# Kernel optimization log

Measured on AMD Instinct MI355X. Metric: run time of the kernel, lower is better.

Reference implementation:

```python
import math
import jax, jax.numpy as jnp
import numpy as np

NUM_HEADS = 12
HEAD_DIM = 64
HIDDEN = NUM_HEADS * HEAD_DIM  # 768
SEQ = 4096


def setup_inputs() -> dict:
    key = jax.random.key(0)
    ks = jax.random.split(key, 7)
    s = 0.02  # BERT-style init scale for weights
    return {
        "hidden_states": jax.random.normal(ks[0], (1, SEQ, HIDDEN), jnp.float32),
        "Wq": jax.random.normal(ks[1], (HIDDEN, HIDDEN), jnp.float32) * s,
        "bq": jax.random.normal(ks[2], (HIDDEN,), jnp.float32) * s,
        "Wk": jax.random.normal(ks[3], (HIDDEN, HIDDEN), jnp.float32) * s,
        "bk": jax.random.normal(ks[4], (HIDDEN,), jnp.float32) * s,
        "Wv": jax.random.normal(ks[5], (HIDDEN, HIDDEN), jnp.float32) * s,
        "bv": jax.random.normal(ks[6], (HIDDEN,), jnp.float32) * s,
    }


def _split_heads(z):
    # [S, HIDDEN] -> [H, S, dh]
    S = z.shape[0]
    return jnp.transpose(z.reshape(S, NUM_HEADS, HEAD_DIM), (1, 0, 2))


def reference(hidden_states, Wq, bq, Wk, bk, Wv, bv):
    # batch is squeezed in the original module (kernel is unbatched)
    x = hidden_states[0]  # [S, D]
    q = _split_heads(x @ Wq.T + bq)  # [H, S, dh]
    k = _split_heads(x @ Wk.T + bk)  # [H, S, dh]
    scale = 1.0 / math.sqrt(HEAD_DIM)
    scores = jnp.einsum('hqd,hkd->hqk', q, k) * scale  # [H, S, S]
    probs = jax.nn.softmax(scores, axis=-1)
    # multi_rand_attn_cuda approximates P @ (x @ Wv^T + bv) via CDF-driven
    # Monte-Carlo column sampling of Wv; its expectation is the exact product,
    # which is the correctness baseline computed here.
    v = _split_heads(x @ Wv.T + bv)  # [H, S, dh]
    ctx = jnp.einsum('hqk,hkd->hqd', probs, v)  # [H, S, dh]
    ctx = jnp.transpose(ctx, (1, 0, 2)).reshape(x.shape[0], HIDDEN)
    return ctx[None]  # [1, S, D]
```

## Files before the change

### kernel.cpp

```cpp
#include <hip/hip_runtime.h>
#include <stdint.h>


typedef float    f32x4 __attribute__((ext_vector_type(4)));
typedef _Float16 h16x8 __attribute__((ext_vector_type(8)));
typedef _Float16 h16x4 __attribute__((ext_vector_type(4)));
typedef _Float16 h16x2 __attribute__((ext_vector_type(2)));
typedef __fp16   fp16x2 __attribute__((ext_vector_type(2)));
typedef unsigned short u16;

#define MFMA32(A, B, C) __builtin_amdgcn_mfma_f32_16x16x32_f16((A), (B), (C), 0, 0, 0)
#define ZERO4 ((f32x4){0.f, 0.f, 0.f, 0.f})

#define SEQ 4096
#define HID 768
#define NH  12
#define DH  64

#define CEXP 0.18033688011112042f

__device__ __forceinline__ u16 f2h(float f) {
  union { _Float16 h; u16 u; } v;
  v.h = (_Float16)f;
  return v.u;
}
__device__ __forceinline__ float h2f(u16 u) {
  union { u16 u; _Float16 h; } v;
  v.u = u;
  return (float)v.h;
}

__device__ __forceinline__ void gload_lds16(const void* g, void* l) {
  __builtin_amdgcn_global_load_lds(
      (__attribute__((address_space(1))) void*)(g),
      (__attribute__((address_space(3))) void*)(l),
      16, 0, 0);
}

__global__ __launch_bounds__(256) void cast_all_k(
    const float* __restrict__ x,  const float* __restrict__ wq,
    const float* __restrict__ wk, const float* __restrict__ wv,
    u16* __restrict__ xh,  u16* __restrict__ wqh,
    u16* __restrict__ wkh, u16* __restrict__ wvh)
{
  int i = blockIdx.x * 256 + threadIdx.x;
  const int NX4 = (SEQ * HID) / 4;
  const int NW4 = (HID * HID) / 4;
  const float4* src; ushort4* dst; int idx;
  if (i < NX4) {
    src = (const float4*)x; dst = (ushort4*)xh; idx = i;
  } else {
    int j = i - NX4;
    int w = j / NW4;
    idx = j - w * NW4;
    src = (const float4*)(w == 0 ? wq : (w == 1 ? wk : wv));
    dst = (ushort4*)(w == 0 ? wqh : (w == 1 ? wkh : wvh));
  }
  float4 v = src[idx];
  ushort4 o;
  o.x = f2h(v.x); o.y = f2h(v.y); o.z = f2h(v.z); o.w = f2h(v.w);
  dst[idx] = o;
}

__global__ __launch_bounds__(256, 3) void qkv_gemm_k(
    const u16* __restrict__ xh,
    const u16* __restrict__ wqh, const u16* __restrict__ wkh, const u16* __restrict__ wvh,
    const float* __restrict__ bq, const float* __restrict__ bk, const float* __restrict__ bv,
    u16* __restrict__ Qh, u16* __restrict__ Kh, u16* __restrict__ Vt)
{
  __shared__ u16 S[128 * 128];

  const int t = threadIdx.x;
  const int wave = t >> 6, lane = t & 63;
  const int m = lane & 15, quad = lane >> 4;
  const int z  = blockIdx.z;
  const int n0 = blockIdx.x * 128;
  const int m0 = blockIdx.y * 128;

  const u16*   W    = (z == 0) ? wqh : (z == 1) ? wkh : wvh;
  const float* bias = (z == 0) ? bq  : (z == 1) ? bk  : bv;

  const int wm = (wave >> 1) * 64;
  const int wn = (wave & 1) * 64;

  f32x4 acc[4][4];
#pragma unroll
  for (int i = 0; i < 4; i++)
#pragma unroll
    for (int j = 0; j < 4; j++) acc[i][j] = ZERO4;

  const int srow = wave * 8 + (lane >> 3);
  const int scg  = (lane & 7) ^ (srow & 7);
  const u16* gA = xh + (m0 + srow) * HID + scg * 8;
  const u16* gB = W  + (n0 + srow) * HID + scg * 8;
  u16* lA = S + wave * 512;
  u16* lB = S + 8192 + wave * 512;

  for (int k0 = 0; k0 < HID; k0 += 64) {
    __syncthreads();
#pragma unroll
    for (int c = 0; c < 4; c++) {
      gload_lds16(gA + c * 32 * HID + k0, lA + c * 2048);
      gload_lds16(gB + c * 32 * HID + k0, lB + c * 2048);
    }
    __syncthreads();

#pragma unroll
    for (int s = 0; s < 2; s++) {
      h16x8 af[4], bf[4];
#pragma unroll
      for (int i = 0; i < 4; i++)
        af[i] = *(const h16x8*)(S + (wm + i * 16 + m) * 64
                                + ((s * 4 + quad) ^ (m & 7)) * 8);
#pragma unroll
      for (int j = 0; j < 4; j++)
        bf[j] = *(const h16x8*)(S + 8192 + (wn + j * 16 + m) * 64
                                + ((s * 4 + quad) ^ (m & 7)) * 8);
#pragma unroll
      for (int i = 0; i < 4; i++)
#pragma unroll
        for (int j = 0; j < 4; j++)
          acc[i][j] = MFMA32(af[i], bf[j], acc[i][j]);
    }
  }

  __syncthreads();

  if (z < 2) {
    const float sc = (z == 0) ? CEXP : 1.0f;
#pragma unroll
    for (int i = 0; i < 4; i++) {
      int sl = wm + i * 16 + quad * 4;
#pragma unroll
      for (int j = 0; j < 4; j++) {
        int colp = wn + j * 16 + m;
        float bb = bias[n0 + colp];
        int c = colp >> 3, sub = colp & 7;
#pragma unroll
        for (int r = 0; r < 4; r++)
          S[(sl + r) * 128 + ((c ^ ((sl + r) & 15)) * 8) + sub] =
              f2h((acc[i][j][r] + bb) * sc);
      }
    }
    __syncthreads();
    u16* outp = (z == 0) ? Qh : Kh;
    const int ch = t & 15;
#pragma unroll
    for (int rr = 0; rr < 8; rr++) {
      int s = rr * 16 + (t >> 4);
      h16x8 v = *(const h16x8*)(S + s * 128 + ((ch ^ (s & 15)) * 8));
      *(h16x8*)(outp + (m0 + s) * HID + n0 + ch * 8) = v;
    }
  } else {
#pragma unroll
    for (int i = 0; i < 4; i++) {
      int sl = wm + i * 16 + quad * 4;
      int vp = (sl & ~31) + ((sl >> 2) & 3) * 8 + ((sl >> 4) & 1) * 4;
#pragma unroll
      for (int j = 0; j < 4; j++) {
        int nl = wn + j * 16 + m;
        float bb = bias[n0 + nl];
        h16x4 o;
        o[0] = (_Float16)(acc[i][j][0] + bb);
        o[1] = (_Float16)(acc[i][j][1] + bb);
        o[2] = (_Float16)(acc[i][j][2] + bb);
        o[3] = (_Float16)(acc[i][j][3] + bb);
        *(h16x4*)(S + nl * 128 + (((vp >> 3) ^ (nl & 15)) * 8) + (vp & 7)) = o;
      }
    }
    __syncthreads();
    const int ch = t & 15;
#pragma unroll
    for (int rr = 0; rr < 8; rr++) {
      int n = rr * 16 + (t >> 4);
      h16x8 v = *(const h16x8*)(S + n * 128 + ((ch ^ (n & 15)) * 8));
      *(h16x8*)(Vt + (n0 + n) * SEQ + m0 + ch * 8) = v;
    }
  }
}

__global__ __launch_bounds__(256, 3) void attn_k(
    const u16* __restrict__ Qh, const u16* __restrict__ Kh, const u16* __restrict__ Vt,
    float* __restrict__ out0, u16* __restrict__ Op1, float* __restrict__ Lp)
{
  __shared__ u16 Ks[128 * 64];
  __shared__ u16 Vs[64 * 128];

  const int t = threadIdx.x;
  const int wave = t >> 6, lane = t & 63;
  const int m = lane & 15, quad = lane >> 4;
  const int h  = blockIdx.y;
  const int q0 = blockIdx.x * 128;
  const int sp = blockIdx.z;
  const int kvbase = sp * 2048;

  h16x8 qf[2][2];
#pragma unroll
  for (int qn = 0; qn < 2; qn++)
#pragma unroll
    for (int ks = 0; ks < 2; ks++)
      qf[qn][ks] = *(const h16x8*)(Qh + (q0 + wave * 32 + qn * 16 + m) * HID
                                   + h * DH + ks * 32 + quad * 8);

  f32x4 O[2][4];
#pragma unroll
  for (int qn = 0; qn < 2; qn++)
#pragma unroll
    for (int jd = 0; jd < 4; jd++) O[qn][jd] = ZERO4;
  float lsum[2] = {0.f, 0.f};

  const int krow_b = wave * 8 + (lane >> 3);
  const int kcl    = lane & 7;
  const int vrow_b = wave * 4 + (lane >> 4);
  const int vcl    = lane & 15;

  for (int it = 0; it < 16; ++it) {
    const int kv0 = kvbase + it * 128;
    __syncthreads();
#pragma unroll
    for (int c = 0; c < 4; c++) {
      int row = c * 32 + krow_b;
      int cg  = kcl ^ (row & 7);
      gload_lds16(Kh + (kv0 + row) * HID + h * DH + cg * 8,
                  Ks + c * 2048 + wave * 512);
      int d  = c * 16 + vrow_b;
      int vg = vcl ^ (d & 15);
      gload_lds16(Vt + (h * DH + d) * SEQ + kv0 + vg * 8,
                  Vs + c * 2048 + wave * 512);
    }
    __syncthreads();

#pragma unroll
    for (int p = 0; p < 4; ++p) {
      const int krow0 = (2 * p) * 16 + m;
      const int krow1 = krow0 + 16;
      h16x8 kb00 = *(const h16x8*)(Ks + krow0 * 64 + ((    quad) ^ (m & 7)) * 8);
      h16x8 kb01 = *(const h16x8*)(Ks + krow0 * 64 + ((4 + quad) ^ (m & 7)) * 8);
      h16x8 kb10 = *(const h16x8*)(Ks + krow1 * 64 + ((    quad) ^ (m & 7)) * 8);
      h16x8 kb11 = *(const h16x8*)(Ks + krow1 * 64 + ((4 + quad) ^ (m & 7)) * 8);

      h16x8 vb[4];
#pragma unroll
      for (int jd = 0; jd < 4; jd++) {
        int d = jd * 16 + m;
        vb[jd] = *(const h16x8*)(Vs + d * 128 + (((p * 4 + quad) ^ m) * 8));
      }

#pragma unroll
      for (int qn = 0; qn < 2; qn++) {
        f32x4 S0 = MFMA32(kb00, qf[qn][0], ZERO4);
        S0       = MFMA32(kb01, qf[qn][1], S0);
        f32x4 S1 = MFMA32(kb10, qf[qn][0], ZERO4);
        S1       = MFMA32(kb11, qf[qn][1], S1);

        float e0 = __builtin_amdgcn_exp2f(S0[0]);
        float e1 = __builtin_amdgcn_exp2f(S0[1]);
        float e2 = __builtin_amdgcn_exp2f(S0[2]);
        float e3 = __builtin_amdgcn_exp2f(S0[3]);
        float e4 = __builtin_amdgcn_exp2f(S1[0]);
        float e5 = __builtin_amdgcn_exp2f(S1[1]);
        float e6 = __builtin_amdgcn_exp2f(S1[2]);
        float e7 = __builtin_amdgcn_exp2f(S1[3]);
        lsum[qn] += ((e0 + e1) + (e2 + e3)) + ((e4 + e5) + (e6 + e7));

        fp16x2 p01 = __builtin_amdgcn_cvt_pkrtz(e0, e1);
        fp16x2 p23 = __builtin_amdgcn_cvt_pkrtz(e2, e3);
        fp16x2 p45 = __builtin_amdgcn_cvt_pkrtz(e4, e5);
        fp16x2 p67 = __builtin_amdgcn_cvt_pkrtz(e6, e7);
        h16x2 q01 = __builtin_bit_cast(h16x2, p01);
        h16x2 q23 = __builtin_bit_cast(h16x2, p23);
        h16x2 q45 = __builtin_bit_cast(h16x2, p45);
        h16x2 q67 = __builtin_bit_cast(h16x2, p67);
        h16x4 pl = __builtin_shufflevector(q01, q23, 0, 1, 2, 3);
        h16x4 ph = __builtin_shufflevector(q45, q67, 0, 1, 2, 3);
        h16x8 pa = __builtin_shufflevector(pl, ph, 0, 1, 2, 3, 4, 5, 6, 7);

#pragma unroll
        for (int jd = 0; jd < 4; jd++)
          O[qn][jd] = MFMA32(pa, vb[jd], O[qn][jd]);
      }
    }
  }

#pragma unroll
  for (int qn = 0; qn < 2; qn++) {
    float v = lsum[qn];
    v += __shfl_xor(v, 16, 64);
    v += __shfl_xor(v, 32, 64);
    if (quad == 0)
      Lp[sp * NH * SEQ + h * SEQ + q0 + wave * 32 + qn * 16 + m] = v;
#pragma unroll
    for (int jd = 0; jd < 4; jd++) {
      int col = h * DH + jd * 16 + m;
#pragma unroll
      for (int r = 0; r < 4; r++) {
        int row = q0 + wave * 32 + qn * 16 + quad * 4 + r;
        if (sp == 0) out0[row * HID + col] = O[qn][jd][r];
        else         Op1[row * HID + col] = f2h(O[qn][jd][r]);
      }
    }
  }
}

__global__ __launch_bounds__(256) void reduce_k(
    float* __restrict__ out, const u16* __restrict__ Op1,
    const float* __restrict__ Lp)
{
  int i = blockIdx.x * 256 + threadIdx.x;
  int s  = i / 192;
  int c4 = i - s * 192;
  int h  = c4 >> 4;
  float L = Lp[h * SEQ + s] + Lp[NH * SEQ + h * SEQ + s];
  float inv = __builtin_amdgcn_rcpf(L);
  float4 a = ((const float4*)out)[i];
  ushort4 b = ((const ushort4*)Op1)[i];
  float4 r;
  r.x = (a.x + h2f(b.x)) * inv;
  r.y = (a.y + h2f(b.y)) * inv;
  r.z = (a.z + h2f(b.z)) * inv;
  r.w = (a.w + h2f(b.w)) * inv;
  ((float4*)out)[i] = r;
}

extern "C" void kernel_launch(void* const* d_in, const int* in_sizes, int n_in,
                              void* d_out, int out_size, void* d_ws, size_t ws_size,
                              hipStream_t stream) {
  const float* x  = (const float*)d_in[0];
  const float* Wq = (const float*)d_in[1];
  const float* bq = (const float*)d_in[2];
  const float* Wk = (const float*)d_in[3];
  const float* bk = (const float*)d_in[4];
  const float* Wv = (const float*)d_in[5];
  const float* bv = (const float*)d_in[6];
  float* out = (float*)d_out;

  char* ws = (char*)d_ws;
  u16* Qh  = (u16*)(ws);
  u16* Kh  = (u16*)(ws + 6291456);
  u16* Vt  = (u16*)(ws + 12582912);
  u16* xh  = (u16*)(ws + 18874368);
  u16* wqh = (u16*)(ws + 25165824);
  u16* wkh = (u16*)(ws + 26345472);
  u16* wvh = (u16*)(ws + 27525120);
  u16*   Op1 = (u16*)(ws + 18874368);
  float* Lp  = (float*)(ws + 25165824);

  cast_all_k<<<4800, 256, 0, stream>>>(x, Wq, Wk, Wv, xh, wqh, wkh, wvh);
  qkv_gemm_k<<<dim3(6, 32, 3), 256, 0, stream>>>(xh, wqh, wkh, wvh,
                                                 bq, bk, bv, Qh, Kh, Vt);
  attn_k<<<dim3(32, NH, 2), 256, 0, stream>>>(Qh, Kh, Vt, out, Op1, Lp);
  reduce_k<<<3072, 256, 0, stream>>>(out, Op1, Lp);
}
```

Measured before the change: 159.0 us.

## Fuse split-KV reduction into attention via atomic last-block combine and XCD-aware block mapping

```diff
diff --git a/kernel.cpp b/kernel.cpp
--- a/kernel.cpp
+++ b/kernel.cpp
@@ -73,9 +73,16 @@
   const int t = threadIdx.x;
   const int wave = t >> 6, lane = t & 63;
   const int m = lane & 15, quad = lane >> 4;
-  const int z  = blockIdx.z;
-  const int n0 = blockIdx.x * 128;
-  const int m0 = blockIdx.y * 128;
+
+  const int bid = blockIdx.x;
+  const int xcd = bid & 7;
+  const int kk  = bid >> 3;
+  const int yt  = xcd * 4 + (kk / 18);
+  const int jj  = kk % 18;
+  const int xt  = jj % 6;
+  const int z   = jj / 6;
+  const int n0 = xt * 128;
+  const int m0 = yt * 128;
 
   const u16*   W    = (z == 0) ? wqh : (z == 1) ? wkh : wvh;
   const float* bias = (z == 0) ? bq  : (z == 1) ? bk  : bv;
@@ -181,18 +188,27 @@
 
 __global__ __launch_bounds__(256, 3) void attn_k(
     const u16* __restrict__ Qh, const u16* __restrict__ Kh, const u16* __restrict__ Vt,
-    float* __restrict__ out0, u16* __restrict__ Op1, float* __restrict__ Lp)
+    float* __restrict__ out0, u16* __restrict__ Op1, float* __restrict__ Lp,
+    int* __restrict__ cnt)
 {
   __shared__ u16 Ks[128 * 64];
   __shared__ u16 Vs[64 * 128];
+  __shared__ int role;
 
   const int t = threadIdx.x;
   const int wave = t >> 6, lane = t & 63;
   const int m = lane & 15, quad = lane >> 4;
-  const int h  = blockIdx.y;
-  const int q0 = blockIdx.x * 128;
-  const int sp = blockIdx.z;
+
+  const int bid = blockIdx.x;
+  const int xcd = bid & 7;
+  const int kk  = bid >> 3;
+  const int hs  = xcd * 3 + (kk >> 5);
+  const int x   = kk & 31;
+  const int h   = hs % NH;
+  const int sp  = hs / NH;
+  const int q0 = x * 128;
   const int kvbase = sp * 2048;
+  const int pair = x * NH + h;
 
   h16x8 qf[2][2];
 #pragma unroll
@@ -282,13 +298,18 @@
     }
   }
 
+  float Lq[2];
 #pragma unroll
   for (int qn = 0; qn < 2; qn++) {
     float v = lsum[qn];
     v += __shfl_xor(v, 16, 64);
     v += __shfl_xor(v, 32, 64);
+    Lq[qn] = v;
     if (quad == 0)
       Lp[sp * NH * SEQ + h * SEQ + q0 + wave * 32 + qn * 16 + m] = v;
+  }
+#pragma unroll
+  for (int qn = 0; qn < 2; qn++)
 #pragma unroll
     for (int jd = 0; jd < 4; jd++) {
       int col = h * DH + jd * 16 + m;
@@ -299,27 +320,40 @@
         else         Op1[row * HID + col] = f2h(O[qn][jd][r]);
       }
     }
-  }
-}
-
-__global__ __launch_bounds__(256) void reduce_k(
-    float* __restrict__ out, const u16* __restrict__ Op1,
-    const float* __restrict__ Lp)
-{
-  int i = blockIdx.x * 256 + threadIdx.x;
-  int s  = i / 192;
-  int c4 = i - s * 192;
-  int h  = c4 >> 4;
-  float L = Lp[h * SEQ + s] + Lp[NH * SEQ + h * SEQ + s];
-  float inv = __builtin_amdgcn_rcpf(L);
-  float4 a = ((const float4*)out)[i];
-  ushort4 b = ((const ushort4*)Op1)[i];
-  float4 r;
-  r.x = (a.x + h2f(b.x)) * inv;
-  r.y = (a.y + h2f(b.y)) * inv;
-  r.z = (a.z + h2f(b.z)) * inv;
-  r.w = (a.w + h2f(b.w)) * inv;
-  ((float4*)out)[i] = r;
+
+  __threadfence();
+  if (t == 0) role = atomicAdd(&cnt[pair], 1);
+  __syncthreads();
+  if (role == 0) return;
+  __threadfence();
+
+  float Lo[2];
+#pragma unroll
+  for (int qn = 0; qn < 2; qn++)
+    Lo[qn] = Lp[(1 - sp) * NH * SEQ + h * SEQ + q0 + wave * 32 + qn * 16 + m];
+
+#pragma unroll
+  for (int qn = 0; qn < 2; qn++) {
+    float invr[4];
+#pragma unroll
+    for (int r = 0; r < 4; r++) {
+      float Ls = __shfl(Lq[qn], quad * 4 + r, 64);
+      float Lr = __shfl(Lo[qn], quad * 4 + r, 64);
+      invr[r] = __builtin_amdgcn_rcpf(Ls + Lr);
+    }
+#pragma unroll
+    for (int jd = 0; jd < 4; jd++) {
+      int col = h * DH + jd * 16 + m;
+#pragma unroll
+      for (int r = 0; r < 4; r++) {
+        int row = q0 + wave * 32 + qn * 16 + quad * 4 + r;
+        float own = (sp == 1) ? h2f(f2h(O[qn][jd][r])) : O[qn][jd][r];
+        float oth = (sp == 0) ? h2f(Op1[row * HID + col])
+                              : out0[row * HID + col];
+        out0[row * HID + col] = (own + oth) * invr[r];
+      }
+    }
+  }
 }
 
 extern "C" void kernel_launch(void* const* d_in, const int* in_sizes, int n_in,
@@ -344,10 +378,11 @@
   u16* wvh = (u16*)(ws + 27525120);
   u16*   Op1 = (u16*)(ws + 18874368);
   float* Lp  = (float*)(ws + 25165824);
+  int*   cnt = (int*)(ws + 25559040);
 
   cast_all_k<<<4800, 256, 0, stream>>>(x, Wq, Wk, Wv, xh, wqh, wkh, wvh);
-  qkv_gemm_k<<<dim3(6, 32, 3), 256, 0, stream>>>(xh, wqh, wkh, wvh,
-                                                 bq, bk, bv, Qh, Kh, Vt);
-  attn_k<<<dim3(32, NH, 2), 256, 0, stream>>>(Qh, Kh, Vt, out, Op1, Lp);
-  reduce_k<<<3072, 256, 0, stream>>>(out, Op1, Lp);
-}
+  qkv_gemm_k<<<576, 256, 0, stream>>>(xh, wqh, wkh, wvh,
+                                      bq, bk, bv, Qh, Kh, Vt);
+  hipMemsetAsync(cnt, 0, 384 * sizeof(int), stream);
+  attn_k<<<768, 256, 0, stream>>>(Qh, Kh, Vt, out, Op1, Lp, cnt);
+}
```

New measurement: 331.6 us. 109% more time.
